# Kernel optimization log

Hardware: AMD Instinct MI355X
Metric: run time of the kernel (lower is better)

## Reference

```python
import jax, jax.numpy as jnp
import numpy as np

D_MODEL = 1024
D_FF = 4096
N_EXPERTS = 8
TOP_K = 2
B, S = 4, 2048


def setup_inputs() -> dict:
    key = jax.random.key(0)
    ks = jax.random.split(key, 6)
    x = jax.random.normal(ks[0], (B, S, D_MODEL), dtype=jnp.float32)
    # router gate: nn.Linear(d_model, num_experts, bias=False), weight [E, D]
    gate_w = jax.random.normal(ks[1], (N_EXPERTS, D_MODEL), dtype=jnp.float32) * 0.01
    # expert MLPs, xavier-uniform init
    lim1 = float(np.sqrt(6.0 / (D_MODEL + D_FF)))
    W1 = jax.random.uniform(ks[2], (N_EXPERTS, D_FF, D_MODEL), minval=-lim1, maxval=lim1, dtype=jnp.float32)
    b1 = jnp.zeros((N_EXPERTS, D_FF), dtype=jnp.float32)
    W2 = jax.random.uniform(ks[3], (N_EXPERTS, D_MODEL, D_FF), minval=-lim1, maxval=lim1, dtype=jnp.float32)
    b2 = jnp.zeros((N_EXPERTS, D_MODEL), dtype=jnp.float32)
    return {"x": x, "gate_w": gate_w, "W1": W1, "b1": b1, "W2": W2, "b2": b2}


def reference(x, gate_w, W1, b1, W2, b2):
    Bb, Ss, D = x.shape
    xt = x.reshape(-1, D)                                  # [N, D]
    # --- router ---
    logits = xt @ gate_w.T                                 # [N, E]
    probs = jax.nn.softmax(logits, axis=-1)
    w_topk, idx = jax.lax.top_k(probs, TOP_K)              # [N, K]
    w_topk = w_topk / (jnp.sum(w_topk, axis=-1, keepdims=True) + 1e-9)
    # dense combine weights: zero for unselected experts    [N, E]
    comb = jnp.sum(jax.nn.one_hot(idx, N_EXPERTS, dtype=xt.dtype) * w_topk[..., None], axis=1)
    # --- experts (dense grouped GEMM over all experts) ---
    h = jnp.einsum('nd,efd->enf', xt, W1) + b1[:, None, :]  # [E, N, ff]
    h = jax.nn.relu(h)                                      # dropout=identity (eval)
    y = jnp.einsum('enf,edf->end', h, W2) + b2[:, None, :]  # [E, N, D]
    # --- weighted scatter/combine ---
    out = jnp.einsum('ne,end->nd', comb, y)                 # [N, D]
    return out.reshape(Bb, Ss, D)
```

## Files before the change

### kernel.cpp

```cpp
#include <hip/hip_runtime.h>
#include <hip/hip_bf16.h>
#include <stdint.h>

#define D_MODEL 1024
#define D_FF    4096
#define N_EXP   8
#define TOPK    2
#define NTOK    8192
#define NASSIGN (NTOK*TOPK)

#define BM 128
#define BN 128
#define BK 64
#define THREADS 256

typedef __bf16 bf16_t;
typedef __attribute__((ext_vector_type(8))) bf16_t bf16x8;
typedef __attribute__((ext_vector_type(4))) float f32x4;
typedef __attribute__((ext_vector_type(8))) unsigned short u16x8;

__device__ __forceinline__ unsigned short f2bf(float f) {
    bf16_t b = (bf16_t)f;
    return __builtin_bit_cast(unsigned short, b);
}

__device__ __forceinline__ void gload_lds16(const void* g, void* l) {
    __builtin_amdgcn_global_load_lds(
        (const __attribute__((address_space(1))) void*)g,
        (__attribute__((address_space(3))) void*)l, 16, 0, 0);
}

__global__ __launch_bounds__(256) void fused_pre_kernel(
        const float* __restrict__ x, const float* __restrict__ gw,
        int* __restrict__ counts, int* __restrict__ ltok, float* __restrict__ lw,
        unsigned short* __restrict__ xb, float* __restrict__ out,
        const float* __restrict__ W1, unsigned short* __restrict__ o1, long n1,
        const float* __restrict__ W2, unsigned short* __restrict__ o2, long n2) {
    int blk = blockIdx.x;
    if (blk < 2048) {
        int w = threadIdx.x >> 6;
        int lane = threadIdx.x & 63;
        int n = blk * 4 + w;
        const float* xr = x + (size_t)n * D_MODEL;
        unsigned short* xbr = xb + (size_t)n * D_MODEL;
        float4 z = make_float4(0.f, 0.f, 0.f, 0.f);
        float4* orow4 = (float4*)(out + (size_t)n * D_MODEL);
        #pragma unroll
        for (int i = 0; i < 4; i++) orow4[lane + i * 64] = z;

        float acc[N_EXP];
        #pragma unroll
        for (int e = 0; e < N_EXP; e++) acc[e] = 0.f;
        #pragma unroll
        for (int i = 0; i < 4; i++) {
            int j = lane + i * 64;
            float4 v = ((const float4*)xr)[j];
            ushort4 o;
            o.x = f2bf(v.x); o.y = f2bf(v.y); o.z = f2bf(v.z); o.w = f2bf(v.w);
            ((ushort4*)xbr)[j] = o;
            int d = j * 4;
            #pragma unroll
            for (int e = 0; e < N_EXP; e++) {
                const float* g = gw + e * D_MODEL + d;
                acc[e] += v.x * g[0] + v.y * g[1] + v.z * g[2] + v.w * g[3];
            }
        }
        #pragma unroll
        for (int e = 0; e < N_EXP; e++) {
            #pragma unroll
            for (int off = 32; off > 0; off >>= 1)
                acc[e] += __shfl_down(acc[e], off);
        }
        if (lane == 0) {
            float mx = acc[0];
            #pragma unroll
            for (int e = 1; e < N_EXP; e++) mx = fmaxf(mx, acc[e]);
            float p[N_EXP];
            float s = 0.f;
            #pragma unroll
            for (int e = 0; e < N_EXP; e++) { p[e] = expf(acc[e] - mx); s += p[e]; }
            float inv = 1.f / s;
            #pragma unroll
            for (int e = 0; e < N_EXP; e++) p[e] *= inv;
            int i0 = 0;
            #pragma unroll
            for (int e = 1; e < N_EXP; e++) if (p[e] > p[i0]) i0 = e;
            int i1 = (i0 == 0) ? 1 : 0;
            #pragma unroll
            for (int e = 0; e < N_EXP; e++) if (e != i0 && p[e] > p[i1]) i1 = e;
            float s2 = p[i0] + p[i1] + 1e-9f;
            float w0 = p[i0] / s2, w1 = p[i1] / s2;
            int pos0 = atomicAdd(&counts[i0], 1);
            ltok[i0 * NTOK + pos0] = n; lw[i0 * NTOK + pos0] = w0;
            int pos1 = atomicAdd(&counts[i1], 1);
            ltok[i1 * NTOK + pos1] = n; lw[i1 * NTOK + pos1] = w1;
        }
    } else {
        long stride = 2048L * 256;
        long q1 = n1 / 8, q2 = n2 / 8;
        for (long i = (long)(blk - 2048) * 256 + threadIdx.x; i < q1 + q2; i += stride) {
            const float4* src; ushort4* dst; long k;
            if (i < q1) { src = (const float4*)W1; dst = (ushort4*)o1; k = i; }
            else        { src = (const float4*)W2; dst = (ushort4*)o2; k = i - q1; }
            float4 v0 = src[2 * k];
            float4 v1 = src[2 * k + 1];
            ushort4 a, b;
            a.x = f2bf(v0.x); a.y = f2bf(v0.y); a.z = f2bf(v0.z); a.w = f2bf(v0.w);
            b.x = f2bf(v1.x); b.y = f2bf(v1.y); b.z = f2bf(v1.z); b.w = f2bf(v1.w);
            dst[2 * k] = a;
            dst[2 * k + 1] = b;
        }
    }
}

__global__ void scan_kernel(const int* __restrict__ counts, int* __restrict__ offs) {
    if (threadIdx.x == 0 && blockIdx.x == 0) {
        int s = 0;
        for (int e = 0; e < N_EXP; e++) { offs[e] = s; s += counts[e]; }
    }
}

__global__ __launch_bounds__(THREADS, 3) void gemm1_kernel(
        const unsigned short* __restrict__ xb, const unsigned short* __restrict__ w1b,
        const float* __restrict__ b1,
        const int* __restrict__ counts, const int* __restrict__ offs,
        const int* __restrict__ ltok,
        unsigned short* __restrict__ hb) {
    const int NTM = NTOK / BM;
    int b = blockIdx.x;
    int e = b & 7;
    int idx = b >> 3;
    int nt = idx / NTM;
    int mt = idx % NTM;
    int cnt = counts[e];
    if (mt * BM >= cnt) return;

    __shared__ __align__(16) unsigned short As[BM * BK];
    __shared__ __align__(16) unsigned short Bs[BN * BK];

    int t = threadIdx.x;
    int lane = t & 63, w = t >> 6;
    int wr = w >> 1, wc = w & 1;

    int srow = t >> 3;
    int schunk = (t & 7) ^ (srow & 7);
    const unsigned short* aptr[4];
    const unsigned short* bptr[4];
    #pragma unroll
    for (int j = 0; j < 4; j++) {
        int rr = srow + j * 32;
        int slot = mt * BM + rr;
        int cs = slot < cnt ? slot : (cnt - 1);
        int tok = ltok[e * NTOK + cs];
        aptr[j] = xb + (size_t)tok * D_MODEL + schunk * 8;
        bptr[j] = w1b + ((size_t)e * D_FF + nt * BN + rr) * D_MODEL + schunk * 8;
    }
    char* As_b = (char*)As;
    char* Bs_b = (char*)Bs;

    int arow_base = wr * 64 + (lane & 15);
    int brow_base = wc * 64 + (lane & 15);
    int ch[2];
    #pragma unroll
    for (int ks = 0; ks < 2; ks++)
        ch[ks] = ((ks * 4 + (lane >> 4)) ^ (lane & 7)) << 4;

    f32x4 acc[4][4];
    #pragma unroll
    for (int m = 0; m < 4; m++)
        #pragma unroll
        for (int n = 0; n < 4; n++)
            acc[m][n] = (f32x4){0.f, 0.f, 0.f, 0.f};

    for (int k0 = 0; k0 < D_MODEL; k0 += BK) {
        #pragma unroll
        for (int j = 0; j < 4; j++) {
            gload_lds16(aptr[j] + k0, As_b + j * 4096 + t * 16);
            gload_lds16(bptr[j] + k0, Bs_b + j * 4096 + t * 16);
        }
        __syncthreads();
        bf16x8 af[2][4], bf[2][4];
        #pragma unroll
        for (int ks = 0; ks < 2; ks++) {
            #pragma unroll
            for (int m = 0; m < 4; m++)
                af[ks][m] = *(const bf16x8*)(As_b + (size_t)(arow_base + m * 16) * 128 + ch[ks]);
            #pragma unroll
            for (int n = 0; n < 4; n++)
                bf[ks][n] = *(const bf16x8*)(Bs_b + (size_t)(brow_base + n * 16) * 128 + ch[ks]);
        }
        #pragma unroll
        for (int ks = 0; ks < 2; ks++)
            #pragma unroll
            for (int m = 0; m < 4; m++)
                #pragma unroll
                for (int n = 0; n < 4; n++)
                    acc[m][n] = __builtin_amdgcn_mfma_f32_16x16x32_bf16(af[ks][m], bf[ks][n], acc[m][n], 0, 0, 0);
        __syncthreads();
    }

    int hbase = offs[e];
    float biasv[4];
    #pragma unroll
    for (int n = 0; n < 4; ++n)
        biasv[n] = b1[e * D_FF + nt * BN + wc * 64 + n * 16 + (lane & 15)];
    unsigned short* Hs = (unsigned short*)(As_b) + w * 1216;
    #pragma unroll
    for (int m = 0; m < 4; ++m) {
        #pragma unroll
        for (int n = 0; n < 4; ++n) {
            #pragma unroll
            for (int rq = 0; rq < 4; ++rq) {
                int lr = (lane >> 4) * 4 + rq;
                int lc = n * 16 + (lane & 15);
                float v = fmaxf(acc[m][n][rq] + biasv[n], 0.f);
                Hs[lr * 72 + lc] = f2bf(v);
            }
        }
        #pragma unroll
        for (int half = 0; half < 2; ++half) {
            int lr = half * 8 + (lane >> 3);
            u16x8 vv = *(const u16x8*)(Hs + lr * 72 + (lane & 7) * 8);
            int s = mt * BM + wr * 64 + m * 16 + lr;
            if (s < cnt) {
                *(u16x8*)(hb + (size_t)(hbase + s) * D_FF + nt * BN + wc * 64 + (lane & 7) * 8) = vv;
            }
        }
    }
}

__global__ __launch_bounds__(THREADS, 3) void gemm2_kernel(
        const unsigned short* __restrict__ hb, const unsigned short* __restrict__ w2b,
        const float* __restrict__ b2,
        const int* __restrict__ counts, const int* __restrict__ offs,
        const int* __restrict__ ltok, const float* __restrict__ lw,
        float* __restrict__ out) {
    const int NTM = NTOK / BM;
    int b = blockIdx.x;
    int e = b & 7;
    int idx = b >> 3;
    int nt = idx / NTM;
    int mt = idx % NTM;
    int cnt = counts[e];
    if (mt * BM >= cnt) return;
    int hbase = offs[e];

    __shared__ __align__(16) unsigned short As[BM * BK];
    __shared__ __align__(16) unsigned short Bs[BN * BK];

    int t = threadIdx.x;
    int lane = t & 63, w = t >> 6;
    int wr = w >> 1, wc = w & 1;

    int srow = t >> 3;
    int schunk = (t & 7) ^ (srow & 7);
    const unsigned short* aptr[4];
    const unsigned short* bptr[4];
    #pragma unroll
    for (int j = 0; j < 4; j++) {
        int rr = srow + j * 32;
        int slot = mt * BM + rr;
        int cs = slot < cnt ? slot : (cnt - 1);
        aptr[j] = hb + (size_t)(hbase + cs) * D_FF + schunk * 8;
        bptr[j] = w2b + ((size_t)e * D_MODEL + nt * BN + rr) * D_FF + schunk * 8;
    }
    char* As_b = (char*)As;
    char* Bs_b = (char*)Bs;

    int arow_base = wr * 64 + (lane & 15);
    int brow_base = wc * 64 + (lane & 15);
    int ch[2];
    #pragma unroll
    for (int ks = 0; ks < 2; ks++)
        ch[ks] = ((ks * 4 + (lane >> 4)) ^ (lane & 7)) << 4;

    f32x4 acc[4][4];
    #pragma unroll
    for (int m = 0; m < 4; m++)
        #pragma unroll
        for (int n = 0; n < 4; n++)
            acc[m][n] = (f32x4){0.f, 0.f, 0.f, 0.f};

    for (int k0 = 0; k0 < D_FF; k0 += BK) {
        #pragma unroll
        for (int j = 0; j < 4; j++) {
            gload_lds16(aptr[j] + k0, As_b + j * 4096 + t * 16);
            gload_lds16(bptr[j] + k0, Bs_b + j * 4096 + t * 16);
        }
        __syncthreads();
        bf16x8 af[2][4], bf[2][4];
        #pragma unroll
        for (int ks = 0; ks < 2; ks++) {
            #pragma unroll
            for (int m = 0; m < 4; m++)
                af[ks][m] = *(const bf16x8*)(As_b + (size_t)(arow_base + m * 16) * 128 + ch[ks]);
            #pragma unroll
            for (int n = 0; n < 4; n++)
                bf[ks][n] = *(const bf16x8*)(Bs_b + (size_t)(brow_base + n * 16) * 128 + ch[ks]);
        }
        #pragma unroll
        for (int ks = 0; ks < 2; ks++)
            #pragma unroll
            for (int m = 0; m < 4; m++)
                #pragma unroll
                for (int n = 0; n < 4; n++)
                    acc[m][n] = __builtin_amdgcn_mfma_f32_16x16x32_bf16(af[ks][m], bf[ks][n], acc[m][n], 0, 0, 0);
        __syncthreads();
    }

    int lbase = e * NTOK;
    float biasv[4];
    #pragma unroll
    for (int n = 0; n < 4; ++n)
        biasv[n] = b2[e * D_MODEL + nt * BN + wc * 64 + n * 16 + (lane & 15)];
    #pragma unroll
    for (int m = 0; m < 4; ++m) {
        int s0 = mt * BM + wr * 64 + m * 16 + (lane >> 4) * 4;
        #pragma unroll
        for (int rq = 0; rq < 4; ++rq) {
            int s = s0 + rq;
            if (s >= cnt) continue;
            int tok = ltok[lbase + s];
            float wgt = lw[lbase + s];
            float* orow = out + (size_t)tok * D_MODEL + nt * BN + wc * 64 + (lane & 15);
            #pragma unroll
            for (int n = 0; n < 4; ++n)
                atomicAdd(orow + n * 16, wgt * (acc[m][n][rq] + biasv[n]));
        }
    }
}

extern "C" void kernel_launch(void* const* d_in, const int* in_sizes, int n_in,
                              void* d_out, int out_size, void* d_ws, size_t ws_size,
                              hipStream_t stream) {
    const float* x  = (const float*)d_in[0];
    const float* gw = (const float*)d_in[1];
    const float* W1 = (const float*)d_in[2];
    const float* b1 = (const float*)d_in[3];
    const float* W2 = (const float*)d_in[4];
    const float* b2 = (const float*)d_in[5];
    float* out = (float*)d_out;

    char* ws = (char*)d_ws;
    size_t off = 0;
    auto alloc = [&](size_t bytes) -> char* {
        char* p = ws + off;
        off += (bytes + 255) & ~(size_t)255;
        return p;
    };
    unsigned short* xb  = (unsigned short*)alloc((size_t)NTOK * D_MODEL * 2);
    unsigned short* w1b = (unsigned short*)alloc((size_t)N_EXP * D_FF * D_MODEL * 2);
    unsigned short* w2b = (unsigned short*)alloc((size_t)N_EXP * D_MODEL * D_FF * 2);
    unsigned short* hb  = (unsigned short*)alloc((size_t)NASSIGN * D_FF * 2);
    int*   counts = (int*)alloc(256);
    int*   offs   = (int*)alloc(256);
    int*   ltok   = (int*)alloc((size_t)N_EXP * NTOK * 4);
    float* lw     = (float*)alloc((size_t)N_EXP * NTOK * 4);

    hipMemsetAsync(counts, 0, 256, stream);
    fused_pre_kernel<<<4096, 256, 0, stream>>>(
        x, gw, counts, ltok, lw, xb, out,
        W1, w1b, (long)N_EXP * D_FF * D_MODEL, W2, w2b, (long)N_EXP * D_MODEL * D_FF);
    scan_kernel<<<1, 64, 0, stream>>>(counts, offs);
    gemm1_kernel<<<N_EXP * (NTOK / BM) * (D_FF / BN), THREADS, 0, stream>>>(
        xb, w1b, b1, counts, offs, ltok, hb);
    gemm2_kernel<<<N_EXP * (NTOK / BM) * (D_MODEL / BN), THREADS, 0, stream>>>(
        hb, w2b, b2, counts, offs, ltok, lw, out);
}
```

Measured before the change: 654.4 us.

## Build expert token lists deterministically with ballot compaction; nontemporal weight conversion

The router no longer does global atomics per token. It writes per-token expert/weight records, and a single-block kernel then compacts them into sorted per-expert lists using wavefront ballots and popcount. That kernel also computes counts and offsets, which removes the memset and the separate scan kernel. The weight fp32-to-bf16 conversion now uses nontemporal loads and stores to avoid polluting the cache. The single-block list builder scans all 16K assignments serially per wave, which adds a small serial latency.

Result: faster. 599.2 us (-8.4%).

```diff
diff --git a/kernel.cpp b/kernel.cpp
--- a/kernel.cpp
+++ b/kernel.cpp
@@ -17,7 +17,9 @@
 typedef __bf16 bf16_t;
 typedef __attribute__((ext_vector_type(8))) bf16_t bf16x8;
 typedef __attribute__((ext_vector_type(4))) float f32x4;
+typedef __attribute__((ext_vector_type(4))) float f32v4;
 typedef __attribute__((ext_vector_type(8))) unsigned short u16x8;
+typedef __attribute__((ext_vector_type(4))) unsigned short u16x4;
 
 __device__ __forceinline__ unsigned short f2bf(float f) {
     bf16_t b = (bf16_t)f;
@@ -32,7 +34,7 @@
 
 __global__ __launch_bounds__(256) void fused_pre_kernel(
         const float* __restrict__ x, const float* __restrict__ gw,
-        int* __restrict__ counts, int* __restrict__ ltok, float* __restrict__ lw,
+        int* __restrict__ recE, float* __restrict__ recW,
         unsigned short* __restrict__ xb, float* __restrict__ out,
         const float* __restrict__ W1, unsigned short* __restrict__ o1, long n1,
         const float* __restrict__ W2, unsigned short* __restrict__ o2, long n2) {
@@ -89,32 +91,48 @@
             #pragma unroll
             for (int e = 0; e < N_EXP; e++) if (e != i0 && p[e] > p[i1]) i1 = e;
             float s2 = p[i0] + p[i1] + 1e-9f;
-            float w0 = p[i0] / s2, w1 = p[i1] / s2;
-            int pos0 = atomicAdd(&counts[i0], 1);
-            ltok[i0 * NTOK + pos0] = n; lw[i0 * NTOK + pos0] = w0;
-            int pos1 = atomicAdd(&counts[i1], 1);
-            ltok[i1 * NTOK + pos1] = n; lw[i1 * NTOK + pos1] = w1;
+            recE[2 * n]     = i0;  recW[2 * n]     = p[i0] / s2;
+            recE[2 * n + 1] = i1;  recW[2 * n + 1] = p[i1] / s2;
         }
     } else {
         long stride = 2048L * 256;
         long q1 = n1 / 8, q2 = n2 / 8;
         for (long i = (long)(blk - 2048) * 256 + threadIdx.x; i < q1 + q2; i += stride) {
-            const float4* src; ushort4* dst; long k;
-            if (i < q1) { src = (const float4*)W1; dst = (ushort4*)o1; k = i; }
-            else        { src = (const float4*)W2; dst = (ushort4*)o2; k = i - q1; }
-            float4 v0 = src[2 * k];
-            float4 v1 = src[2 * k + 1];
-            ushort4 a, b;
+            const f32v4* src; u16x4* dst; long k;
+            if (i < q1) { src = (const f32v4*)W1; dst = (u16x4*)o1; k = i; }
+            else        { src = (const f32v4*)W2; dst = (u16x4*)o2; k = i - q1; }
+            f32v4 v0 = __builtin_nontemporal_load(src + 2 * k);
+            f32v4 v1 = __builtin_nontemporal_load(src + 2 * k + 1);
+            u16x4 a, b;
             a.x = f2bf(v0.x); a.y = f2bf(v0.y); a.z = f2bf(v0.z); a.w = f2bf(v0.w);
             b.x = f2bf(v1.x); b.y = f2bf(v1.y); b.z = f2bf(v1.z); b.w = f2bf(v1.w);
-            dst[2 * k] = a;
-            dst[2 * k + 1] = b;
-        }
-    }
-}
-
-__global__ void scan_kernel(const int* __restrict__ counts, int* __restrict__ offs) {
-    if (threadIdx.x == 0 && blockIdx.x == 0) {
+            __builtin_nontemporal_store(a, dst + 2 * k);
+            __builtin_nontemporal_store(b, dst + 2 * k + 1);
+        }
+    }
+}
+
+__global__ __launch_bounds__(512) void build_lists_kernel(
+        const int* __restrict__ recE, const float* __restrict__ recW,
+        int* __restrict__ counts, int* __restrict__ offs,
+        int* __restrict__ ltok, float* __restrict__ lw) {
+    int we = threadIdx.x >> 6;
+    int lane = threadIdx.x & 63;
+    int base = 0;
+    for (int j0 = 0; j0 < NASSIGN; j0 += 64) {
+        int e = recE[j0 + lane];
+        float wt = recW[j0 + lane];
+        unsigned long long m = __ballot(e == we);
+        if (e == we) {
+            int pos = base + __builtin_popcountll(m & ((1ull << lane) - 1));
+            ltok[we * NTOK + pos] = (j0 + lane) >> 1;
+            lw[we * NTOK + pos] = wt;
+        }
+        base += __builtin_popcountll(m);
+    }
+    if (lane == 0) counts[we] = base;
+    __syncthreads();
+    if (threadIdx.x == 0) {
         int s = 0;
         for (int e = 0; e < N_EXP; e++) { offs[e] = s; s += counts[e]; }
     }
@@ -356,12 +374,13 @@
     int*   offs   = (int*)alloc(256);
     int*   ltok   = (int*)alloc((size_t)N_EXP * NTOK * 4);
     float* lw     = (float*)alloc((size_t)N_EXP * NTOK * 4);
-
-    hipMemsetAsync(counts, 0, 256, stream);
+    int*   recE   = (int*)alloc((size_t)NASSIGN * 4);
+    float* recW   = (float*)alloc((size_t)NASSIGN * 4);
+
     fused_pre_kernel<<<4096, 256, 0, stream>>>(
-        x, gw, counts, ltok, lw, xb, out,
+        x, gw, recE, recW, xb, out,
         W1, w1b, (long)N_EXP * D_FF * D_MODEL, W2, w2b, (long)N_EXP * D_MODEL * D_FF);
-    scan_kernel<<<1, 64, 0, stream>>>(counts, offs);
+    build_lists_kernel<<<1, 512, 0, stream>>>(recE, recW, counts, offs, ltok, lw);
     gemm1_kernel<<<N_EXP * (NTOK / BM) * (D_FF / BN), THREADS, 0, stream>>>(
         xb, w1b, b1, counts, offs, ltok, hb);
     gemm2_kernel<<<N_EXP * (NTOK / BM) * (D_MODEL / BN), THREADS, 0, stream>>>(
```
